# Kernel tuning notes

Measured on AMD Instinct MI355X. Metric: run time of the kernel, lower is better.

The kernel has to match this reference:

```python
import jax, jax.numpy as jnp
import numpy as np

EPS = 1e-6
NUM_HEADS = 4
GSIZE = (2, 2, 2)


def _ln_channels_first(x, w, b):
    # LayerNorm over channel dim (axis=1) of [B,C,D,H,W]
    u = x.mean(1, keepdims=True)
    s = ((x - u) ** 2).mean(1, keepdims=True)
    xn = (x - u) / jnp.sqrt(s + EPS)
    return w[None, :, None, None, None] * xn + b[None, :, None, None, None]


def setup_inputs() -> dict:
    key = jax.random.key(0)
    ks = jax.random.split(key, 7)
    B, C = 2, 256
    x2 = jax.random.normal(ks[0], (B, C, 32, 32, 32), jnp.float32)
    x1_low = jax.random.normal(ks[1], (B, C, 16, 16, 16), jnp.float32)
    sc = 1.0 / np.sqrt(C).astype(np.float32)
    q_w = jax.random.normal(ks[2], (C, C), jnp.float32) * sc
    k_w = jax.random.normal(ks[3], (C, C), jnp.float32) * sc
    v_w = jax.random.normal(ks[4], (C, C), jnp.float32) * sc
    dw_w = jax.random.normal(ks[5], (C, 1, 3, 3, 3), jnp.float32) * (1.0 / np.sqrt(27.0).astype(np.float32))
    proj_w = jax.random.normal(ks[6], (C, C), jnp.float32) * sc
    nq_w = jnp.ones((C,), jnp.float32)
    nq_b = jnp.zeros((C,), jnp.float32)
    nkv_w = jnp.ones((C,), jnp.float32)
    nkv_b = jnp.zeros((C,), jnp.float32)
    return {"x2": x2, "x1_low": x1_low, "q_w": q_w, "k_w": k_w, "v_w": v_w,
            "dw_w": dw_w, "proj_w": proj_w, "nq_w": nq_w, "nq_b": nq_b,
            "nkv_w": nkv_w, "nkv_b": nkv_b}


def reference(x2, x1_low, q_w, k_w, v_w, dw_w, proj_w, nq_w, nq_b, nkv_w, nkv_b):
    B, C, D, H, W = x2.shape
    h = NUM_HEADS
    d = C // h
    gD, gH, gW = GSIZE
    _, _, Dl, Hl, Wl = x1_low.shape

    # adaptive_avg_pool3d to (gD,gH,gW): dims divisible -> block means
    tokens = x1_low.reshape(B, C, gD, Dl // gD, gH, Hl // gH, gW, Wl // gW).mean((3, 5, 7))
    # depthwise 3x3x3 conv, padding 1
    dw = jax.lax.conv_general_dilated(
        tokens, dw_w, window_strides=(1, 1, 1), padding='SAME',
        dimension_numbers=('NCDHW', 'OIDHW', 'NCDHW'), feature_group_count=C)
    tokens = tokens + dw

    N = D * H * W
    g = gD * gH * gW

    qx = _ln_channels_first(x2, nq_w, nq_b).reshape(B, C, N)
    q = jnp.einsum('oc,bcn->bon', q_w, qx).reshape(B, h, d, N).transpose(0, 1, 3, 2)  # [B,h,N,d]

    tk = _ln_channels_first(tokens, nkv_w, nkv_b).reshape(B, C, g)
    k = jnp.einsum('oc,bcg->bog', k_w, tk).reshape(B, h, d, g)  # [B,h,d,g]
    v = jnp.einsum('oc,bcg->bog', v_w, tokens.reshape(B, C, g)).reshape(B, h, d, g).transpose(0, 1, 3, 2)  # [B,h,g,d]

    attn = jax.nn.softmax(jnp.einsum('bhnd,bhdg->bhng', q, k) / jnp.sqrt(jnp.float32(d)), axis=-1)
    out = jnp.einsum('bhng,bhgd->bhnd', attn, v)  # [B,h,N,d]
    out = out.transpose(0, 1, 3, 2).reshape(B, C, N)
    return jnp.einsum('oc,bcn->bon', proj_w, out).reshape(B, C, D, H, W)
```

## Files before the change

kernel.cpp:

```cpp
#include <hip/hip_runtime.h>
#include <math.h>

#define EPS 1e-6f

typedef __attribute__((ext_vector_type(8))) short bhalf8;
typedef __attribute__((ext_vector_type(4))) float floatx4;

__device__ __forceinline__ unsigned short f2bf(float f) {
    union { float f; unsigned u; } v; v.f = f;
    unsigned r = (v.u + 0x7fffu + ((v.u >> 16) & 1u)) >> 16;
    return (unsigned short)r;
}
__device__ __forceinline__ float bflo(unsigned u) {
    union { unsigned x; float f; } v; v.x = u << 16; return v.f;
}
__device__ __forceinline__ float bfhi(unsigned u) {
    union { unsigned x; float f; } v; v.x = u & 0xffff0000u; return v.f;
}

__global__ void prep_weights(const float* __restrict__ q_w,
                             const float* __restrict__ proj_w,
                             const float* __restrict__ nq_w,
                             const float* __restrict__ nq_b,
                             float* __restrict__ W1, float* __restrict__ W2,
                             unsigned short* __restrict__ W1b,
                             unsigned short* __restrict__ W2b,
                             float* __restrict__ A, float* __restrict__ Bc) {
    int o = blockIdx.x;
    int c = threadIdx.x;
    float qv = q_w[o * 256 + c];
    float pv = proj_w[o * 256 + c];
    float w1 = qv * nq_w[c];
    W1[c * 256 + o] = w1;
    W2[c * 256 + o] = pv;
    int kc = c >> 5, kk = c & 31;
    W1b[kc * 8192 + o * 32 + kk] = f2bf(w1);
    W2b[kc * 8192 + o * 32 + kk] = f2bf(pv);
    float bcv = qv * nq_b[c];
    __shared__ float sA[4], sB[4];
    float a = w1, b = bcv;
    for (int off = 32; off > 0; off >>= 1) {
        a += __shfl_down(a, off);
        b += __shfl_down(b, off);
    }
    int wave = threadIdx.x >> 6, lane = threadIdx.x & 63;
    if (lane == 0) { sA[wave] = a; sB[wave] = b; }
    __syncthreads();
    if (threadIdx.x == 0) {
        A[o]  = sA[0] + sA[1] + sA[2] + sA[3];
        Bc[o] = sB[0] + sB[1] + sB[2] + sB[3];
    }
}

__global__ void pool_tokens(const float* __restrict__ x1, float* __restrict__ tokens) {
    int bc = blockIdx.x;
    const float* base = x1 + (size_t)bc * 4096;
    int wave = threadIdx.x >> 6;
    int lane = threadIdx.x & 63;
    int doff = lane >> 3, hoff = lane & 7;
    for (int t = wave * 2; t < wave * 2 + 2; ++t) {
        int gd = t >> 2, gh = (t >> 1) & 1, gw = t & 1;
        const float* p = base + (gd * 8 + doff) * 256 + (gh * 8 + hoff) * 16 + gw * 8;
        float4 v0 = *(const float4*)p;
        float4 v1 = *(const float4*)(p + 4);
        float s = v0.x + v0.y + v0.z + v0.w + v1.x + v1.y + v1.z + v1.w;
        for (int off = 32; off > 0; off >>= 1) s += __shfl_down(s, off);
        if (lane == 0) tokens[bc * 8 + t] = s * (1.0f / 512.0f);
    }
}

__global__ void tokens_kv(const float* __restrict__ tokens,
                          const float* __restrict__ dw_w,
                          const float* __restrict__ k_w,
                          const float* __restrict__ v_w,
                          const float* __restrict__ nkv_w,
                          const float* __restrict__ nkv_b,
                          float* __restrict__ kk, float* __restrict__ vv,
                          unsigned short* __restrict__ kkb) {
    int b = blockIdx.x;
    int c = threadIdx.x;
    __shared__ float t2[256][8];
    __shared__ float u8[8], r8[8];
    float t[8];
    #pragma unroll
    for (int g = 0; g < 8; ++g) t[g] = tokens[(b * 256 + c) * 8 + g];
    float w[27];
    #pragma unroll
    for (int i = 0; i < 27; ++i) w[i] = dw_w[c * 27 + i];
    #pragma unroll
    for (int z = 0; z < 2; ++z)
    #pragma unroll
    for (int y = 0; y < 2; ++y)
    #pragma unroll
    for (int x = 0; x < 2; ++x) {
        float s = 0.f;
        #pragma unroll
        for (int i = 0; i < 3; ++i) {
            int nz = z + i - 1; if (nz < 0 || nz > 1) continue;
            #pragma unroll
            for (int j = 0; j < 3; ++j) {
                int ny = y + j - 1; if (ny < 0 || ny > 1) continue;
                #pragma unroll
                for (int l = 0; l < 3; ++l) {
                    int nx = x + l - 1; if (nx < 0 || nx > 1) continue;
                    s += w[(i * 3 + j) * 3 + l] * t[nz * 4 + ny * 2 + nx];
                }
            }
        }
        int g = z * 4 + y * 2 + x;
        t2[c][g] = t[g] + s;
    }
    __syncthreads();
    if (c < 8) {
        float su = 0.f, sq = 0.f;
        for (int cc = 0; cc < 256; ++cc) { float v = t2[cc][c]; su += v; sq += v * v; }
        float u = su * (1.f / 256.f);
        float var = sq * (1.f / 256.f) - u * u;
        u8[c] = u;
        r8[c] = rsqrtf(var + EPS);
    }
    __syncthreads();
    int o = c;
    float acck[8] = {0,0,0,0,0,0,0,0}, accv[8] = {0,0,0,0,0,0,0,0};
    for (int cc = 0; cc < 256; ++cc) {
        float kwv = k_w[o * 256 + cc];
        float vwv = v_w[o * 256 + cc];
        float nw = nkv_w[cc], nb = nkv_b[cc];
        #pragma unroll
        for (int g = 0; g < 8; ++g) {
            float tv = t2[cc][g];
            float tn = nw * (tv - u8[g]) * r8[g] + nb;
            acck[g] += kwv * tn;
            accv[g] += vwv * tv;
        }
    }
    int h = o >> 6, d = o & 63;
    #pragma unroll
    for (int g = 0; g < 8; ++g) {
        int ki = ((b * 4 + h) * 64 + d) * 8 + g;
        int vi = ((b * 4 + h) * 8 + g) * 64 + d;
        kk[ki] = acck[g];
        vv[vi] = accv[g];
        kkb[ki] = f2bf(acck[g]);
    }
}

__global__ void ln_stats(const float* __restrict__ x2,
                         float* __restrict__ u, float* __restrict__ r) {
    int t = blockIdx.x * blockDim.x + threadIdx.x;
    int n = t << 2;
    int b = n >> 15;
    int pos = n & 32767;
    const float* p = x2 + (size_t)b * 8388608 + pos;
    float su0 = 0, su1 = 0, su2 = 0, su3 = 0;
    float sq0 = 0, sq1 = 0, sq2 = 0, sq3 = 0;
    for (int c = 0; c < 256; ++c) {
        float4 v = *(const float4*)(p + (size_t)c * 32768);
        su0 += v.x; sq0 += v.x * v.x;
        su1 += v.y; sq1 += v.y * v.y;
        su2 += v.z; sq2 += v.z * v.z;
        su3 += v.w; sq3 += v.w * v.w;
    }
    const float inv = 1.f / 256.f;
    float4 um, rm;
    um.x = su0 * inv; um.y = su1 * inv; um.z = su2 * inv; um.w = su3 * inv;
    rm.x = rsqrtf(sq0 * inv - um.x * um.x + EPS);
    rm.y = rsqrtf(sq1 * inv - um.y * um.y + EPS);
    rm.z = rsqrtf(sq2 * inv - um.z * um.z + EPS);
    rm.w = rsqrtf(sq3 * inv - um.w * um.w + EPS);
    *(float4*)(u + n) = um;
    *(float4*)(r + n) = rm;
}

__global__ __launch_bounds__(256, 2)
void fused_mfma(const float* __restrict__ x2,
                const unsigned short* __restrict__ W1b,
                const unsigned short* __restrict__ W2b,
                const float* __restrict__ Ag, const float* __restrict__ Bg,
                const unsigned short* __restrict__ kkb,
                const float* __restrict__ vvf,
                float* __restrict__ out) {
    __shared__ unsigned short XQ[16896];
    __shared__ unsigned short ks[2048];
    __shared__ float vs[2048];
    __shared__ float part[16][64][2];
    __shared__ float As[256], Bs[256], us[64], rs[64];

    const int tid = threadIdx.x;
    const int w = tid >> 6;
    const int lane = tid & 63;
    const int n0g = blockIdx.x * 64;
    const int b = n0g >> 15;

    ((uint4*)ks)[tid] = ((const uint4*)(kkb + b * 2048))[tid];
    ((float4*)vs)[tid]       = ((const float4*)(vvf + b * 2048))[tid];
    ((float4*)vs)[256 + tid] = ((const float4*)(vvf + b * 2048))[256 + tid];
    As[tid] = Ag[tid];
    Bs[tid] = Bg[tid];

    {
        const int n4 = tid & 15, cg = tid >> 4;
        const float* xb = x2 + (size_t)b * 8388608 + (n0g & 32767) + n4 * 4;
        float su[4] = {0,0,0,0}, sq[4] = {0,0,0,0};
        #pragma unroll
        for (int cc = 0; cc < 8; ++cc) {
            int p = cg + 16 * cc;
            int c0 = 2 * p;
            float4 a  = *(const float4*)(xb + (size_t)c0 * 32768);
            float4 bq = *(const float4*)(xb + (size_t)(c0 + 1) * 32768);
            int g = p >> 2, wsub = p & 3;
            float av[4] = {a.x, a.y, a.z, a.w};
            float bv[4] = {bq.x, bq.y, bq.z, bq.w};
            #pragma unroll
            for (int i = 0; i < 4; ++i) {
                su[i] += av[i] + bv[i];
                sq[i] += av[i] * av[i] + bv[i] * bv[i];
                int row = 4 * n4 + i;
                int swz = ((row >> 2) ^ row) & 7;
                unsigned val = (unsigned)f2bf(av[i]) | ((unsigned)f2bf(bv[i]) << 16);
                ((unsigned*)XQ)[row * 128 + ((g ^ swz) << 2) + wsub] = val;
            }
        }
        #pragma unroll
        for (int i = 0; i < 4; ++i) {
            part[cg][4 * n4 + i][0] = su[i];
            part[cg][4 * n4 + i][1] = sq[i];
        }
    }
    __syncthreads();
    if (tid < 64) {
        float S = 0, Q = 0;
        #pragma unroll
        for (int gg = 0; gg < 16; ++gg) { S += part[gg][tid][0]; Q += part[gg][tid][1]; }
        float mu = S * (1.f / 256.f);
        us[tid] = mu;
        rs[tid] = rsqrtf(Q * (1.f / 256.f) - mu * mu + EPS);
    }

    const int m = lane & 15;
    const int qd = lane >> 4;

    floatx4 acc[4][4];
    #pragma unroll
    for (int i = 0; i < 4; ++i)
        #pragma unroll
        for (int j = 0; j < 4; ++j)
            acc[i][j] = (floatx4){0.f, 0.f, 0.f, 0.f};

    const unsigned short* w1p = W1b + (size_t)((4 * w) * 16 + m) * 32 + qd * 8;
    {
        bhalf8 afb[2][4];
        #pragma unroll
        for (int t = 0; t < 4; ++t) afb[0][t] = *(const bhalf8*)(w1p + t * 512);
        #pragma unroll
        for (int kc = 0; kc < 8; ++kc) {
            if (kc < 7) {
                #pragma unroll
                for (int t = 0; t < 4; ++t)
                    afb[(kc + 1) & 1][t] = *(const bhalf8*)(w1p + (kc + 1) * 8192 + t * 512);
            }
            bhalf8 bfr[4];
            #pragma unroll
            for (int nt = 0; nt < 4; ++nt) {
                int n = nt * 16 + m;
                int swz = ((n >> 2) ^ n) & 7;
                bfr[nt] = *(const bhalf8*)(XQ + n * 256 + (((4 * kc + qd) ^ swz) << 3));
            }
            #pragma unroll
            for (int t = 0; t < 4; ++t)
                #pragma unroll
                for (int nt = 0; nt < 4; ++nt)
                    acc[t][nt] = __builtin_amdgcn_mfma_f32_16x16x32_bf16(afb[kc & 1][t], bfr[nt], acc[t][nt], 0, 0, 0);
        }
    }
    __syncthreads();

    #pragma unroll
    for (int t = 0; t < 4; ++t) {
        int ob = 64 * w + 16 * t + 4 * qd;
        floatx4 Af = *(const floatx4*)&As[ob];
        floatx4 Bf = *(const floatx4*)&Bs[ob];
        #pragma unroll
        for (int nt = 0; nt < 4; ++nt) {
            int n = nt * 16 + m;
            float uv = us[n], rv = rs[n];
            unsigned p0 = (unsigned)f2bf(rv * (acc[t][nt][0] - uv * Af[0]) + Bf[0])
                        | ((unsigned)f2bf(rv * (acc[t][nt][1] - uv * Af[1]) + Bf[1]) << 16);
            unsigned p1 = (unsigned)f2bf(rv * (acc[t][nt][2] - uv * Af[2]) + Bf[2])
                        | ((unsigned)f2bf(rv * (acc[t][nt][3] - uv * Af[3]) + Bf[3]) << 16);
            uint2 val; val.x = p0; val.y = p1;
            *(uint2*)(XQ + n * 264 + ob) = val;
        }
    }

    {
        unsigned short* qrow = XQ + lane * 264 + w * 64;
        uint4 q4[8];
        #pragma unroll
        for (int j = 0; j < 8; ++j) q4[j] = *(const uint4*)(qrow + j * 8);
        float lg[8] = {0, 0, 0, 0, 0, 0, 0, 0};
        const unsigned short* kh = ks + w * 512;
        #pragma unroll
        for (int dp = 0; dp < 32; ++dp) {
            unsigned qq = ((const unsigned*)q4)[dp];
            float q0 = bflo(qq), q1 = bfhi(qq);
            uint4 k0 = *(const uint4*)(kh + dp * 16);
            uint4 k1 = *(const uint4*)(kh + dp * 16 + 8);
            lg[0] += q0 * bflo(k0.x); lg[1] += q0 * bfhi(k0.x);
            lg[2] += q0 * bflo(k0.y); lg[3] += q0 * bfhi(k0.y);
            lg[4] += q0 * bflo(k0.z); lg[5] += q0 * bfhi(k0.z);
            lg[6] += q0 * bflo(k0.w); lg[7] += q0 * bfhi(k0.w);
            lg[0] += q1 * bflo(k1.x); lg[1] += q1 * bfhi(k1.x);
            lg[2] += q1 * bflo(k1.y); lg[3] += q1 * bfhi(k1.y);
            lg[4] += q1 * bflo(k1.z); lg[5] += q1 * bfhi(k1.z);
            lg[6] += q1 * bflo(k1.w); lg[7] += q1 * bfhi(k1.w);
        }
        float mx = lg[0];
        #pragma unroll
        for (int g = 1; g < 8; ++g) mx = fmaxf(mx, lg[g]);
        float p[8], s = 0.f;
        #pragma unroll
        for (int g = 0; g < 8; ++g) { p[g] = __expf((lg[g] - mx) * 0.125f); s += p[g]; }
        float is = 1.f / s;
        #pragma unroll
        for (int g = 0; g < 8; ++g) p[g] *= is;
        float o2[64];
        #pragma unroll
        for (int j = 0; j < 64; ++j) o2[j] = 0.f;
        const float* vh = vs + w * 512;
        #pragma unroll
        for (int g = 0; g < 8; ++g) {
            float pg = p[g];
            #pragma unroll
            for (int j = 0; j < 16; ++j) {
                float4 vv4 = *(const float4*)(vh + g * 64 + j * 4);
                o2[4 * j + 0] += pg * vv4.x;
                o2[4 * j + 1] += pg * vv4.y;
                o2[4 * j + 2] += pg * vv4.z;
                o2[4 * j + 3] += pg * vv4.w;
            }
        }
        #pragma unroll
        for (int j = 0; j < 8; ++j) {
            uint4 pk;
            pk.x = (unsigned)f2bf(o2[8 * j + 0]) | ((unsigned)f2bf(o2[8 * j + 1]) << 16);
            pk.y = (unsigned)f2bf(o2[8 * j + 2]) | ((unsigned)f2bf(o2[8 * j + 3]) << 16);
            pk.z = (unsigned)f2bf(o2[8 * j + 4]) | ((unsigned)f2bf(o2[8 * j + 5]) << 16);
            pk.w = (unsigned)f2bf(o2[8 * j + 6]) | ((unsigned)f2bf(o2[8 * j + 7]) << 16);
            *(uint4*)(qrow + j * 8) = pk;
        }
    }
    __syncthreads();

    floatx4 acc2[4][4];
    #pragma unroll
    for (int i = 0; i < 4; ++i)
        #pragma unroll
        for (int j = 0; j < 4; ++j)
            acc2[i][j] = (floatx4){0.f, 0.f, 0.f, 0.f};

    const unsigned short* w2p = W2b + (size_t)((4 * w) * 16 + m) * 32 + qd * 8;
    {
        bhalf8 afb[2][4];
        #pragma unroll
        for (int t = 0; t < 4; ++t) afb[0][t] = *(const bhalf8*)(w2p + t * 512);
        #pragma unroll
        for (int kc = 0; kc < 8; ++kc) {
            if (kc < 7) {
                #pragma unroll
                for (int t = 0; t < 4; ++t)
                    afb[(kc + 1) & 1][t] = *(const bhalf8*)(w2p + (kc + 1) * 8192 + t * 512);
            }
            bhalf8 bfr[4];
            #pragma unroll
            for (int nt = 0; nt < 4; ++nt) {
                int n = nt * 16 + m;
                bfr[nt] = *(const bhalf8*)(XQ + n * 264 + kc * 32 + qd * 8);
            }
            #pragma unroll
            for (int t = 0; t < 4; ++t)
                #pragma unroll
                for (int nt = 0; nt < 4; ++nt)
                    acc2[t][nt] = __builtin_amdgcn_mfma_f32_16x16x32_bf16(afb[kc & 1][t], bfr[nt], acc2[t][nt], 0, 0, 0);
        }
    }

    float* ob = out + (size_t)b * 8388608 + (n0g & 32767);
    #pragma unroll
    for (int t = 0; t < 4; ++t) {
        int o0 = 64 * w + 16 * t + 4 * qd;
        #pragma unroll
        for (int nt = 0; nt < 4; ++nt) {
            int n = nt * 16 + m;
            #pragma unroll
            for (int rr = 0; rr < 4; ++rr)
                ob[(size_t)(o0 + rr) * 32768 + n] = acc2[t][nt][rr];
        }
    }
}

#define TN 64
#define KC 16
#define QP 68

__global__ __launch_bounds__(256, 1)
void fused_main(const float* __restrict__ x2,
                const float* __restrict__ W1,
                const float* __restrict__ W2,
                const float* __restrict__ Avec,
                const float* __restrict__ Bvec,
                const float* __restrict__ uarr,
                const float* __restrict__ rarr,
                const float* __restrict__ kk,
                const float* __restrict__ vv,
                float* __restrict__ out) {
    __shared__ __align__(16) float wsm[KC * 256];
    __shared__ __align__(16) float xs[KC][72];
    __shared__ __align__(16) float qs[256][QP];
    __shared__ __align__(16) float ksm[4 * 64 * 8];
    __shared__ __align__(16) float vsm[4 * 8 * 64];

    int tid = threadIdx.x;
    int n0g = blockIdx.x * TN;
    int b = n0g >> 15;
    int pos0 = n0g & 32767;
    const float* x2b = x2 + (size_t)b * 8388608 + pos0;

    {
        const float4* kkb4 = (const float4*)(kk + b * 2048);
        const float4* vvb4 = (const float4*)(vv + b * 2048);
        for (int i = tid; i < 512; i += 256) {
            ((float4*)ksm)[i] = kkb4[i];
            ((float4*)vsm)[i] = vvb4[i];
        }
    }

    int ty = tid >> 3;
    int tx = tid & 7;
    float acc[8][8];
    #pragma unroll
    for (int i = 0; i < 8; ++i)
        #pragma unroll
        for (int j = 0; j < 8; ++j) acc[i][j] = 0.f;

    for (int kc = 0; kc < 256; kc += KC) {
        __syncthreads();
        {
            const float4* src = (const float4*)(W1 + kc * 256);
            float4* dst = (float4*)wsm;
            #pragma unroll
            for (int i = 0; i < 4; ++i) dst[tid + 256 * i] = src[tid + 256 * i];
        }
        {
            int kr = tid >> 4;
            int j4 = tid & 15;
            float4 v = *(const float4*)(x2b + (size_t)(kc + kr) * 32768 + j4 * 4);
            *(float4*)&xs[kr][j4 * 4] = v;
        }
        __syncthreads();
        #pragma unroll
        for (int k = 0; k < KC; ++k) {
            float a[8], bb[8];
            *(float4*)&a[0]  = *(float4*)&wsm[k * 256 + 8 * ty];
            *(float4*)&a[4]  = *(float4*)&wsm[k * 256 + 8 * ty + 4];
            *(float4*)&bb[0] = *(float4*)&xs[k][8 * tx];
            *(float4*)&bb[4] = *(float4*)&xs[k][8 * tx + 4];
            #pragma unroll
            for (int i = 0; i < 8; ++i)
                #pragma unroll
                for (int j = 0; j < 8; ++j)
                    acc[i][j] += a[i] * bb[j];
        }
    }

    {
        float uv[8], rv[8], Ai[8], Bi[8];
        #pragma unroll
        for (int j = 0; j < 8; ++j) { uv[j] = uarr[n0g + 8 * tx + j]; rv[j] = rarr[n0g + 8 * tx + j]; }
        #pragma unroll
        for (int i = 0; i < 8; ++i) { Ai[i] = Avec[8 * ty + i]; Bi[i] = Bvec[8 * ty + i]; }
        #pragma unroll
        for (int i = 0; i < 8; ++i)
            #pragma unroll
            for (int j = 0; j < 8; ++j)
                qs[8 * ty + i][8 * tx + j] = rv[j] * (acc[i][j] - uv[j] * Ai[i]) + Bi[i];
    }
    __syncthreads();

    {
        int n = tid & 63;
        int h = tid >> 6;
        const float* ksh = ksm + h * 512;
        const float* vsh = vsm + h * 512;
        float logit[8];
        #pragma unroll
        for (int g = 0; g < 8; ++g) logit[g] = 0.f;
        for (int d = 0; d < 64; ++d) {
            float qv = qs[h * 64 + d][n];
            #pragma unroll
            for (int g = 0; g < 8; ++g) logit[g] += qv * ksh[d * 8 + g];
        }
        float mm = logit[0];
        #pragma unroll
        for (int g = 1; g < 8; ++g) mm = fmaxf(mm, logit[g]);
        float p[8], s = 0.f;
        #pragma unroll
        for (int g = 0; g < 8; ++g) { p[g] = __expf((logit[g] - mm) * 0.125f); s += p[g]; }
        float pinv = 1.f / s;
        #pragma unroll
        for (int g = 0; g < 8; ++g) p[g] *= pinv;
        for (int d = 0; d < 64; ++d) {
            float ov = 0.f;
            #pragma unroll
            for (int g = 0; g < 8; ++g) ov += p[g] * vsh[g * 64 + d];
            qs[h * 64 + d][n] = ov;
        }
    }

    float acc2[8][8];
    #pragma unroll
    for (int i = 0; i < 8; ++i)
        #pragma unroll
        for (int j = 0; j < 8; ++j) acc2[i][j] = 0.f;

    for (int kc = 0; kc < 256; kc += KC) {
        __syncthreads();
        {
            const float4* src = (const float4*)(W2 + kc * 256);
            float4* dst = (float4*)wsm;
            #pragma unroll
            for (int i = 0; i < 4; ++i) dst[tid + 256 * i] = src[tid + 256 * i];
        }
        __syncthreads();
        #pragma unroll
        for (int k = 0; k < KC; ++k) {
            float a[8], bb[8];
            *(float4*)&a[0]  = *(float4*)&wsm[k * 256 + 8 * ty];
            *(float4*)&a[4]  = *(float4*)&wsm[k * 256 + 8 * ty + 4];
            *(float4*)&bb[0] = *(float4*)&qs[kc + k][8 * tx];
            *(float4*)&bb[4] = *(float4*)&qs[kc + k][8 * tx + 4];
            #pragma unroll
            for (int i = 0; i < 8; ++i)
                #pragma unroll
                for (int j = 0; j < 8; ++j)
                    acc2[i][j] += a[i] * bb[j];
        }
    }

    float* ob = out + (size_t)b * 8388608 + pos0;
    #pragma unroll
    for (int i = 0; i < 8; ++i) {
        float* row = ob + (size_t)(8 * ty + i) * 32768 + 8 * tx;
        *(float4*)row       = *(float4*)&acc2[i][0];
        *(float4*)(row + 4) = *(float4*)&acc2[i][4];
    }
}

extern "C" void kernel_launch(void* const* d_in, const int* in_sizes, int n_in,
                              void* d_out, int out_size, void* d_ws, size_t ws_size,
                              hipStream_t stream) {
    (void)in_sizes; (void)n_in; (void)out_size;
    const float* x2     = (const float*)d_in[0];
    const float* x1_low = (const float*)d_in[1];
    const float* q_w    = (const float*)d_in[2];
    const float* k_w    = (const float*)d_in[3];
    const float* v_w    = (const float*)d_in[4];
    const float* dw_w   = (const float*)d_in[5];
    const float* proj_w = (const float*)d_in[6];
    const float* nq_w   = (const float*)d_in[7];
    const float* nq_b   = (const float*)d_in[8];
    const float* nkv_w  = (const float*)d_in[9];
    const float* nkv_b  = (const float*)d_in[10];
    float* outp = (float*)d_out;

    float* wsf = (float*)d_ws;
    float* W1f = wsf;
    float* W2f = wsf + 65536;
    float* Av  = wsf + 131072;
    float* Bv  = wsf + 131328;
    float* u   = wsf + 131584;
    float* r   = wsf + 197120;
    float* tk  = wsf + 262656;
    float* kkf = wsf + 266752;
    float* vvf = wsf + 270848;
    unsigned short* W1b = (unsigned short*)(wsf + 274944);
    unsigned short* W2b = (unsigned short*)(wsf + 307712);
    unsigned short* kkb = (unsigned short*)(wsf + 340480);
    const size_t need_bytes = (size_t)341504 * 4;

    prep_weights<<<256, 256, 0, stream>>>(q_w, proj_w, nq_w, nq_b, W1f, W2f, W1b, W2b, Av, Bv);
    pool_tokens<<<512, 256, 0, stream>>>(x1_low, tk);
    tokens_kv<<<2, 256, 0, stream>>>(tk, dw_w, k_w, v_w, nkv_w, nkv_b, kkf, vvf, kkb);

    if (ws_size >= need_bytes) {
        fused_mfma<<<1024, 256, 0, stream>>>(x2, W1b, W2b, Av, Bv, kkb, vvf, outp);
    } else {
        ln_stats<<<64, 256, 0, stream>>>(x2, u, r);
        fused_main<<<1024, 256, 0, stream>>>(x2, W1f, W2f, Av, Bv, u, r, kkf, vvf, outp);
    }
}
```

Baseline: 199.1 us.

## Restructure preprocessing kernels and shrink fused kernel LDS for higher occupancy

Merges the weight-prep and token-pool kernels into one launch. The old 2-block token projection is split into a normalize kernel and a 128-block projection kernel that uses wave reductions, so the serial 256-step loop becomes parallel. In the main fused kernel, LDS shrinks by reusing the LN-partials buffer for K/V (held in registers until after the stats pass) and dropping row padding in favour of an XOR swizzle. Launch bounds rise to 3 blocks per SM. The risks are register pressure under the tighter launch bound and one extra barrier.

```diff
diff --git a/kernel.cpp b/kernel.cpp
--- a/kernel.cpp
+++ b/kernel.cpp
@@ -18,65 +18,63 @@
     union { unsigned x; float f; } v; v.x = u & 0xffff0000u; return v.f;
 }
 
-__global__ void prep_weights(const float* __restrict__ q_w,
-                             const float* __restrict__ proj_w,
-                             const float* __restrict__ nq_w,
-                             const float* __restrict__ nq_b,
-                             float* __restrict__ W1, float* __restrict__ W2,
-                             unsigned short* __restrict__ W1b,
-                             unsigned short* __restrict__ W2b,
-                             float* __restrict__ A, float* __restrict__ Bc) {
-    int o = blockIdx.x;
-    int c = threadIdx.x;
-    float qv = q_w[o * 256 + c];
-    float pv = proj_w[o * 256 + c];
-    float w1 = qv * nq_w[c];
-    W1[c * 256 + o] = w1;
-    W2[c * 256 + o] = pv;
-    int kc = c >> 5, kk = c & 31;
-    W1b[kc * 8192 + o * 32 + kk] = f2bf(w1);
-    W2b[kc * 8192 + o * 32 + kk] = f2bf(pv);
-    float bcv = qv * nq_b[c];
-    __shared__ float sA[4], sB[4];
-    float a = w1, b = bcv;
-    for (int off = 32; off > 0; off >>= 1) {
-        a += __shfl_down(a, off);
-        b += __shfl_down(b, off);
-    }
-    int wave = threadIdx.x >> 6, lane = threadIdx.x & 63;
-    if (lane == 0) { sA[wave] = a; sB[wave] = b; }
-    __syncthreads();
-    if (threadIdx.x == 0) {
-        A[o]  = sA[0] + sA[1] + sA[2] + sA[3];
-        Bc[o] = sB[0] + sB[1] + sB[2] + sB[3];
-    }
-}
-
-__global__ void pool_tokens(const float* __restrict__ x1, float* __restrict__ tokens) {
-    int bc = blockIdx.x;
-    const float* base = x1 + (size_t)bc * 4096;
-    int wave = threadIdx.x >> 6;
-    int lane = threadIdx.x & 63;
-    int doff = lane >> 3, hoff = lane & 7;
-    for (int t = wave * 2; t < wave * 2 + 2; ++t) {
-        int gd = t >> 2, gh = (t >> 1) & 1, gw = t & 1;
-        const float* p = base + (gd * 8 + doff) * 256 + (gh * 8 + hoff) * 16 + gw * 8;
-        float4 v0 = *(const float4*)p;
-        float4 v1 = *(const float4*)(p + 4);
-        float s = v0.x + v0.y + v0.z + v0.w + v1.x + v1.y + v1.z + v1.w;
-        for (int off = 32; off > 0; off >>= 1) s += __shfl_down(s, off);
-        if (lane == 0) tokens[bc * 8 + t] = s * (1.0f / 512.0f);
-    }
-}
-
-__global__ void tokens_kv(const float* __restrict__ tokens,
-                          const float* __restrict__ dw_w,
-                          const float* __restrict__ k_w,
-                          const float* __restrict__ v_w,
-                          const float* __restrict__ nkv_w,
-                          const float* __restrict__ nkv_b,
-                          float* __restrict__ kk, float* __restrict__ vv,
-                          unsigned short* __restrict__ kkb) {
+__global__ void pre1(const float* __restrict__ q_w,
+                     const float* __restrict__ proj_w,
+                     const float* __restrict__ nq_w,
+                     const float* __restrict__ nq_b,
+                     float* __restrict__ W1, float* __restrict__ W2,
+                     unsigned short* __restrict__ W1b,
+                     unsigned short* __restrict__ W2b,
+                     float* __restrict__ A, float* __restrict__ Bc,
+                     const float* __restrict__ x1, float* __restrict__ tokens) {
+    if (blockIdx.x < 256) {
+        int o = blockIdx.x;
+        int c = threadIdx.x;
+        float qv = q_w[o * 256 + c];
+        float pv = proj_w[o * 256 + c];
+        float w1 = qv * nq_w[c];
+        W1[c * 256 + o] = w1;
+        W2[c * 256 + o] = pv;
+        int kc = c >> 5, kk = c & 31;
+        W1b[kc * 8192 + o * 32 + kk] = f2bf(w1);
+        W2b[kc * 8192 + o * 32 + kk] = f2bf(pv);
+        float bcv = qv * nq_b[c];
+        __shared__ float sA[4], sB[4];
+        float a = w1, b = bcv;
+        for (int off = 32; off > 0; off >>= 1) {
+            a += __shfl_down(a, off);
+            b += __shfl_down(b, off);
+        }
+        int wave = threadIdx.x >> 6, lane = threadIdx.x & 63;
+        if (lane == 0) { sA[wave] = a; sB[wave] = b; }
+        __syncthreads();
+        if (threadIdx.x == 0) {
+            A[o]  = sA[0] + sA[1] + sA[2] + sA[3];
+            Bc[o] = sB[0] + sB[1] + sB[2] + sB[3];
+        }
+    } else {
+        int bc = blockIdx.x - 256;
+        const float* base = x1 + (size_t)bc * 4096;
+        int wave = threadIdx.x >> 6;
+        int lane = threadIdx.x & 63;
+        int doff = lane >> 3, hoff = lane & 7;
+        for (int t = wave * 2; t < wave * 2 + 2; ++t) {
+            int gd = t >> 2, gh = (t >> 1) & 1, gw = t & 1;
+            const float* p = base + (gd * 8 + doff) * 256 + (gh * 8 + hoff) * 16 + gw * 8;
+            float4 v0 = *(const float4*)p;
+            float4 v1 = *(const float4*)(p + 4);
+            float s = v0.x + v0.y + v0.z + v0.w + v1.x + v1.y + v1.z + v1.w;
+            for (int off = 32; off > 0; off >>= 1) s += __shfl_down(s, off);
+            if (lane == 0) tokens[bc * 8 + t] = s * (1.0f / 512.0f);
+        }
+    }
+}
+
+__global__ void tokens_prep(const float* __restrict__ tokens,
+                            const float* __restrict__ dw_w,
+                            const float* __restrict__ nkv_w,
+                            const float* __restrict__ nkv_b,
+                            float* __restrict__ t2g, float* __restrict__ tng) {
     int b = blockIdx.x;
     int c = threadIdx.x;
     __shared__ float t2[256][8];
@@ -120,28 +118,58 @@
         r8[c] = rsqrtf(var + EPS);
     }
     __syncthreads();
-    int o = c;
+    float nw = nkv_w[c], nb = nkv_b[c];
+    #pragma unroll
+    for (int g = 0; g < 8; ++g) {
+        float tv = t2[c][g];
+        t2g[(b * 256 + c) * 8 + g] = tv;
+        tng[(b * 256 + c) * 8 + g] = nw * (tv - u8[g]) * r8[g] + nb;
+    }
+}
+
+__global__ void tokens_proj(const float* __restrict__ k_w,
+                            const float* __restrict__ v_w,
+                            const float* __restrict__ t2g,
+                            const float* __restrict__ tng,
+                            float* __restrict__ kk, float* __restrict__ vv,
+                            unsigned short* __restrict__ kkb) {
+    int b = blockIdx.x >> 6;
+    int og = blockIdx.x & 63;
+    int w = threadIdx.x >> 6;
+    int lane = threadIdx.x & 63;
+    int o = og * 4 + w;
     float acck[8] = {0,0,0,0,0,0,0,0}, accv[8] = {0,0,0,0,0,0,0,0};
-    for (int cc = 0; cc < 256; ++cc) {
-        float kwv = k_w[o * 256 + cc];
-        float vwv = v_w[o * 256 + cc];
-        float nw = nkv_w[cc], nb = nkv_b[cc];
+    #pragma unroll
+    for (int i = 0; i < 4; ++i) {
+        int c = lane + 64 * i;
+        float kw = k_w[o * 256 + c];
+        float vw = v_w[o * 256 + c];
+        const float* tb = t2g + (size_t)(b * 256 + c) * 8;
+        const float* nb = tng + (size_t)(b * 256 + c) * 8;
+        float4 ta0 = *(const float4*)tb;
+        float4 ta1 = *(const float4*)(tb + 4);
+        float4 tn0 = *(const float4*)nb;
+        float4 tn1 = *(const float4*)(nb + 4);
+        acck[0] += kw * tn0.x; acck[1] += kw * tn0.y; acck[2] += kw * tn0.z; acck[3] += kw * tn0.w;
+        acck[4] += kw * tn1.x; acck[5] += kw * tn1.y; acck[6] += kw * tn1.z; acck[7] += kw * tn1.w;
+        accv[0] += vw * ta0.x; accv[1] += vw * ta0.y; accv[2] += vw * ta0.z; accv[3] += vw * ta0.w;
+        accv[4] += vw * ta1.x; accv[5] += vw * ta1.y; accv[6] += vw * ta1.z; accv[7] += vw * ta1.w;
+    }
+    #pragma unroll
+    for (int g = 0; g < 8; ++g)
+        for (int off = 32; off > 0; off >>= 1) {
+            acck[g] += __shfl_down(acck[g], off);
+            accv[g] += __shfl_down(accv[g], off);
+        }
+    if (lane == 0) {
         #pragma unroll
         for (int g = 0; g < 8; ++g) {
-            float tv = t2[cc][g];
-            float tn = nw * (tv - u8[g]) * r8[g] + nb;
-            acck[g] += kwv * tn;
-            accv[g] += vwv * tv;
-        }
-    }
-    int h = o >> 6, d = o & 63;
-    #pragma unroll
-    for (int g = 0; g < 8; ++g) {
-        int ki = ((b * 4 + h) * 64 + d) * 8 + g;
-        int vi = ((b * 4 + h) * 8 + g) * 64 + d;
-        kk[ki] = acck[g];
-        vv[vi] = accv[g];
-        kkb[ki] = f2bf(acck[g]);
+            int ki = b * 2048 + o * 8 + g;
+            int vi = b * 2048 + (o >> 6) * 512 + g * 64 + (o & 63);
+            kk[ki] = acck[g];
+            kkb[ki] = f2bf(acck[g]);
+            vv[vi] = accv[g];
+        }
     }
 }
 
@@ -172,7 +200,7 @@
     *(float4*)(r + n) = rm;
 }
 
-__global__ __launch_bounds__(256, 2)
+__global__ __launch_bounds__(256, 3)
 void fused_mfma(const float* __restrict__ x2,
                 const unsigned short* __restrict__ W1b,
                 const unsigned short* __restrict__ W2b,
@@ -180,10 +208,8 @@
                 const unsigned short* __restrict__ kkb,
                 const float* __restrict__ vvf,
                 float* __restrict__ out) {
-    __shared__ unsigned short XQ[16896];
-    __shared__ unsigned short ks[2048];
-    __shared__ float vs[2048];
-    __shared__ float part[16][64][2];
+    __shared__ __align__(16) unsigned short XQ[16384];
+    __shared__ __align__(16) float KVP[3072];
     __shared__ float As[256], Bs[256], us[64], rs[64];
 
     const int tid = threadIdx.x;
@@ -192,9 +218,9 @@
     const int n0g = blockIdx.x * 64;
     const int b = n0g >> 15;
 
-    ((uint4*)ks)[tid] = ((const uint4*)(kkb + b * 2048))[tid];
-    ((float4*)vs)[tid]       = ((const float4*)(vvf + b * 2048))[tid];
-    ((float4*)vs)[256 + tid] = ((const float4*)(vvf + b * 2048))[256 + tid];
+    uint4  kreg  = ((const uint4*)(kkb + b * 2048))[tid];
+    float4 vreg0 = ((const float4*)(vvf + b * 2048))[tid];
+    float4 vreg1 = ((const float4*)(vvf + b * 2048))[256 + tid];
     As[tid] = Ag[tid];
     Bs[tid] = Bg[tid];
 
@@ -223,19 +249,25 @@
         }
         #pragma unroll
         for (int i = 0; i < 4; ++i) {
-            part[cg][4 * n4 + i][0] = su[i];
-            part[cg][4 * n4 + i][1] = sq[i];
+            KVP[cg * 128 + (4 * n4 + i) * 2]     = su[i];
+            KVP[cg * 128 + (4 * n4 + i) * 2 + 1] = sq[i];
         }
     }
     __syncthreads();
     if (tid < 64) {
         float S = 0, Q = 0;
         #pragma unroll
-        for (int gg = 0; gg < 16; ++gg) { S += part[gg][tid][0]; Q += part[gg][tid][1]; }
+        for (int gg = 0; gg < 16; ++gg) { S += KVP[gg * 128 + tid * 2]; Q += KVP[gg * 128 + tid * 2 + 1]; }
         float mu = S * (1.f / 256.f);
         us[tid] = mu;
         rs[tid] = rsqrtf(Q * (1.f / 256.f) - mu * mu + EPS);
     }
+    __syncthreads();
+    unsigned short* ks = (unsigned short*)KVP;
+    float* vs = KVP + 1024;
+    ((uint4*)ks)[tid] = kreg;
+    ((float4*)vs)[tid] = vreg0;
+    ((float4*)vs)[256 + tid] = vreg1;
 
     const int m = lane & 15;
     const int qd = lane >> 4;
@@ -280,24 +312,28 @@
         int ob = 64 * w + 16 * t + 4 * qd;
         floatx4 Af = *(const floatx4*)&As[ob];
         floatx4 Bf = *(const floatx4*)&Bs[ob];
+        int gq = ob >> 3, off = ob & 7;
         #pragma unroll
         for (int nt = 0; nt < 4; ++nt) {
             int n = nt * 16 + m;
+            int swz = ((n >> 2) ^ n) & 7;
             float uv = us[n], rv = rs[n];
             unsigned p0 = (unsigned)f2bf(rv * (acc[t][nt][0] - uv * Af[0]) + Bf[0])
                         | ((unsigned)f2bf(rv * (acc[t][nt][1] - uv * Af[1]) + Bf[1]) << 16);
             unsigned p1 = (unsigned)f2bf(rv * (acc[t][nt][2] - uv * Af[2]) + Bf[2])
                         | ((unsigned)f2bf(rv * (acc[t][nt][3] - uv * Af[3]) + Bf[3]) << 16);
             uint2 val; val.x = p0; val.y = p1;
-            *(uint2*)(XQ + n * 264 + ob) = val;
+            *(uint2*)(XQ + n * 256 + ((gq ^ swz) << 3) + off) = val;
         }
     }
 
     {
-        unsigned short* qrow = XQ + lane * 264 + w * 64;
+        const int sw = ((lane >> 2) ^ lane) & 7;
+        unsigned short* qrow = XQ + lane * 256;
         uint4 q4[8];
         #pragma unroll
-        for (int j = 0; j < 8; ++j) q4[j] = *(const uint4*)(qrow + j * 8);
+        for (int gl = 0; gl < 8; ++gl)
+            q4[gl] = *(const uint4*)(qrow + ((8 * w + (gl ^ sw)) << 3));
         float lg[8] = {0, 0, 0, 0, 0, 0, 0, 0};
         const unsigned short* kh = ks + w * 512;
         #pragma unroll
@@ -341,13 +377,13 @@
             }
         }
         #pragma unroll
-        for (int j = 0; j < 8; ++j) {
+        for (int gl = 0; gl < 8; ++gl) {
             uint4 pk;
-            pk.x = (unsigned)f2bf(o2[8 * j + 0]) | ((unsigned)f2bf(o2[8 * j + 1]) << 16);
-            pk.y = (unsigned)f2bf(o2[8 * j + 2]) | ((unsigned)f2bf(o2[8 * j + 3]) << 16);
-            pk.z = (unsigned)f2bf(o2[8 * j + 4]) | ((unsigned)f2bf(o2[8 * j + 5]) << 16);
-            pk.w = (unsigned)f2bf(o2[8 * j + 6]) | ((unsigned)f2bf(o2[8 * j + 7]) << 16);
-            *(uint4*)(qrow + j * 8) = pk;
+            pk.x = (unsigned)f2bf(o2[8 * gl + 0]) | ((unsigned)f2bf(o2[8 * gl + 1]) << 16);
+            pk.y = (unsigned)f2bf(o2[8 * gl + 2]) | ((unsigned)f2bf(o2[8 * gl + 3]) << 16);
+            pk.z = (unsigned)f2bf(o2[8 * gl + 4]) | ((unsigned)f2bf(o2[8 * gl + 5]) << 16);
+            pk.w = (unsigned)f2bf(o2[8 * gl + 6]) | ((unsigned)f2bf(o2[8 * gl + 7]) << 16);
+            *(uint4*)(qrow + ((8 * w + (gl ^ sw)) << 3)) = pk;
         }
     }
     __syncthreads();
@@ -375,7 +411,8 @@
             #pragma unroll
             for (int nt = 0; nt < 4; ++nt) {
                 int n = nt * 16 + m;
-                bfr[nt] = *(const bhalf8*)(XQ + n * 264 + kc * 32 + qd * 8);
+                int swz = ((n >> 2) ^ n) & 7;
+                bfr[nt] = *(const bhalf8*)(XQ + n * 256 + (((4 * kc + qd) ^ swz) << 3));
             }
             #pragma unroll
             for (int t = 0; t < 4; ++t)
@@ -586,11 +623,14 @@
     unsigned short* W1b = (unsigned short*)(wsf + 274944);
     unsigned short* W2b = (unsigned short*)(wsf + 307712);
     unsigned short* kkb = (unsigned short*)(wsf + 340480);
-    const size_t need_bytes = (size_t)341504 * 4;
-
-    prep_weights<<<256, 256, 0, stream>>>(q_w, proj_w, nq_w, nq_b, W1f, W2f, W1b, W2b, Av, Bv);
-    pool_tokens<<<512, 256, 0, stream>>>(x1_low, tk);
-    tokens_kv<<<2, 256, 0, stream>>>(tk, dw_w, k_w, v_w, nkv_w, nkv_b, kkf, vvf, kkb);
+    float* t2g = wsf + 342528;
+    float* tng = wsf + 346624;
+    const size_t need_bytes = (size_t)350720 * 4;
+
+    pre1<<<768, 256, 0, stream>>>(q_w, proj_w, nq_w, nq_b, W1f, W2f, W1b, W2b, Av, Bv,
+                                  x1_low, tk);
+    tokens_prep<<<2, 256, 0, stream>>>(tk, dw_w, nkv_w, nkv_b, t2g, tng);
+    tokens_proj<<<128, 256, 0, stream>>>(k_w, v_w, t2g, tng, kkf, vvf, kkb);
 
     if (ws_size >= need_bytes) {
         fused_mfma<<<1024, 256, 0, stream>>>(x2, W1b, W2b, Av, Bv, kkb, vvf, outp);
```

Result: faster. 190.7 us (-4.2%).
